# Kernel tuning notes

Measured on AMD Instinct MI355X. Metric: run time of the kernel, lower is better.

## Reference

```python
import jax, jax.numpy as jnp
import numpy as np

EPISODES = 1_000_000


def setup_inputs() -> dict:
    key = jax.random.key(0)
    x = jax.random.normal(key, (1, EPISODES, 2), dtype=jnp.float32)
    return {"x": x}


def _rx_2x2(t):
    # expm(-i * t * X) = cos(t) I - i sin(t) X  (closed form for Pauli-X rotation)
    c = jnp.cos(t).astype(jnp.complex64)
    s = (-1j * jnp.sin(t).astype(jnp.complex64))
    row0 = jnp.stack([c, s], axis=-1)
    row1 = jnp.stack([s, c], axis=-1)
    return jnp.stack([row0, row1], axis=-2)  # (..., 2, 2)


def reference(x):
    # x: (1, E, 2) float32 -> angles a (qubit 1, X(x)I) and b (qubit 2, I(x)X)
    cnot = jnp.array([[1, 0, 0, 0],
                      [0, 1, 0, 0],
                      [0, 0, 0, 1],
                      [0, 0, 1, 0]], dtype=jnp.complex64)
    a = x[..., 0]  # (1, E)
    b = x[..., 1]  # (1, E)
    # sx1 = X(x)I and sx2 = I(x)X commute, so
    # expm(-i (a*sx1 + b*sx2)) = Rx(a) (x) Rx(b)  -- exact, replaces generic expm.
    Ra = _rx_2x2(a)  # (1, E, 2, 2)
    Rb = _rx_2x2(b)  # (1, E, 2, 2)
    # Kronecker product -> (1, E, 4, 4) complex64
    Rx = (Ra[..., :, None, :, None] * Rb[..., None, :, None, :]).reshape(
        a.shape[0], a.shape[1], 4, 4)
    propagator = jnp.einsum('iq,beqp->beip', cnot, Rx)  # (1, E, 4, 4)
    state_out = propagator[..., 0]                      # column 0 -> (1, E, 4)
    probabilities = jnp.square(jnp.abs(state_out)).astype(jnp.float32)
    logits = jnp.log(probabilities)                     # tf.log(prob) for multinomial
    # Vectorized categorical sampling over all episodes (replaces per-episode loop)
    skey = jax.random.key(42)
    choice = jax.random.categorical(skey, logits, axis=-1)  # (1, E) int
    # original: one_hot((1,1)) stacked on axis=1 -> (1, E, 1, 4)
    measurement = jax.nn.one_hot(choice, 4, dtype=jnp.float32)[:, :, None, :]
    return measurement
```

## Files before the change

kernel.cpp:

```cpp
#include <hip/hip_runtime.h>
#include <stdint.h>
#include <math.h>


#define N_EP 1000000

typedef float v2f __attribute__((ext_vector_type(2)));
#define V2(c) ((v2f){(c), (c)})

__device__ __forceinline__ uint32_t rotl32(uint32_t x, int d) {
  return (x << d) | (x >> (32 - d));
}

__device__ __forceinline__ void threefry(uint32_t x0, uint32_t x1,
                                         uint32_t& o0, uint32_t& o1) {
  const uint32_t k0 = 0u;
  const uint32_t k1 = 42u;
  const uint32_t k2 = (0u ^ 42u ^ 0x1BD11BDAu);
  x0 += k0; x1 += k1;
#define R4A { x0 += x1; x1 = rotl32(x1,13); x1 ^= x0; \
              x0 += x1; x1 = rotl32(x1,15); x1 ^= x0; \
              x0 += x1; x1 = rotl32(x1,26); x1 ^= x0; \
              x0 += x1; x1 = rotl32(x1, 6); x1 ^= x0; }
#define R4B { x0 += x1; x1 = rotl32(x1,17); x1 ^= x0; \
              x0 += x1; x1 = rotl32(x1,29); x1 ^= x0; \
              x0 += x1; x1 = rotl32(x1,16); x1 ^= x0; \
              x0 += x1; x1 = rotl32(x1,24); x1 ^= x0; }
  R4A; x0 += k1; x1 += k2 + 1u;
  R4B; x0 += k2; x1 += k0 + 2u;
  R4A; x0 += k0; x1 += k1 + 3u;
  R4B; x0 += k1; x1 += k2 + 4u;
  R4A; x0 += k2; x1 += k0 + 5u;
#undef R4A
#undef R4B
  o0 = x0; o1 = x1;
}

__device__ __forceinline__ v2f logf_xla2(v2f input) {
#pragma clang fp contract(off)
  const float kMinNorm = __uint_as_float(0x00800000u);
  uint32_t ubx = __float_as_uint(fmaxf(input.x, kMinNorm));
  uint32_t uby = __float_as_uint(fmaxf(input.y, kMinNorm));
  v2f e;
  e.x = (float)((int)(ubx >> 23) - 126);
  e.y = (float)((int)(uby >> 23) - 126);
  v2f x;
  x.x = __uint_as_float((ubx & 0x807fffffu) | 0x3f000000u);
  x.y = __uint_as_float((uby & 0x807fffffu) | 0x3f000000u);
  const float kSqrtHf = 0.707106781186547524f;
  bool mx = x.x < kSqrtHf;
  bool my = x.y < kSqrtHf;
  v2f tmp;
  tmp.x = mx ? x.x : 0.0f;
  tmp.y = my ? x.y : 0.0f;
  e.x = e.x - (mx ? 1.0f : 0.0f);
  e.y = e.y - (my ? 1.0f : 0.0f);
  x = x - V2(1.0f);
  x = x + tmp;
  v2f z = x * x;
  v2f y = V2(7.0376836292E-2f);
  y = y * x + V2(-1.1514610310E-1f);
  y = y * x + V2( 1.1676998740E-1f);
  y = y * x + V2(-1.2420140846E-1f);
  y = y * x + V2( 1.4249322787E-1f);
  y = y * x + V2(-1.6668057665E-1f);
  y = y * x + V2( 2.0000714765E-1f);
  y = y * x + V2(-2.4999993993E-1f);
  y = y * x + V2( 3.3333331174E-1f);
  y = y * x;
  y = y * z;
  y = e * V2(-2.12194440e-4f) + y;
  y = z * V2(-0.5f) + y;
  x = x + y;
  x = e * V2(0.693359375f) + x;
  if (input.x == 0.0f) x.x = -__builtin_inff();
  if (input.y == 0.0f) x.y = -__builtin_inff();
  return x;
}

__device__ __forceinline__ void sincosf_cr(float xf, float* sp, float* cp) {
  double x = (double)xf;
  double dn = __builtin_rint(x * 6.36619772367581382433e-01);
  int q = (int)dn;
  const double pio2_1  = 1.57079632673412561417e+00;
  const double pio2_1t = 6.07710050650619224932e-11;
  double r = fma(-dn, pio2_1, x);
  r = fma(-dn, pio2_1t, r);
  double z = r * r;
  double w = z * z;
  const double S1 = -1.66666666666666324348e-01;
  const double S2 =  8.33333333332248946124e-03;
  const double S3 = -1.98412698298579493134e-04;
  const double S4 =  2.75573137070700676789e-06;
  const double S5 = -2.50507602534068634195e-08;
  const double S6 =  1.58969099521155010221e-10;
  double rs = S2 + z * (S3 + z * S4) + z * w * (S5 + z * S6);
  double sinr = r + r * (z * (S1 + z * rs));
  const double C1 =  4.16666666666666019037e-02;
  const double C2 = -1.38888888888741095749e-03;
  const double C3 =  2.48015872894767294178e-05;
  const double C4 = -2.75573143513906633035e-07;
  const double C5 =  2.08757232129817482790e-09;
  const double C6 = -1.13596475577881948265e-11;
  double rc = z * (C1 + z * (C2 + z * C3)) + w * w * (C4 + z * (C5 + z * C6));
  double hz = 0.5 * z;
  double ww = 1.0 - hz;
  double cosr = ww + (((1.0 - ww) - hz) + z * rc);
  bool swap = q & 1;
  double s0 = swap ? cosr : sinr;
  double c0 = swap ? sinr : cosr;
  if (q & 2) s0 = -s0;
  if ((q + 1) & 2) c0 = -c0;
  *sp = (float)s0;
  *cp = (float)c0;
}

__device__ __forceinline__ v2f u2_from_bits(uint32_t b0, uint32_t b1) {
#pragma clang fp contract(off)
  const float tiny = 1.17549435e-38f;
  v2f f;
  f.x = __uint_as_float((b0 >> 9) | 0x3F800000u);
  f.y = __uint_as_float((b1 >> 9) | 0x3F800000u);
  f = f - V2(1.0f);
  f = f + V2(tiny);
  v2f u;
  u.x = fmaxf(tiny, f.x);
  u.y = fmaxf(tiny, f.y);
  return u;
}

__device__ __forceinline__ v2f gumbel2(uint32_t b0, uint32_t b1) {
  v2f u = u2_from_bits(b0, b1);
  v2f inner = logf_xla2(u);
  v2f outer = logf_xla2(-inner);
  return -outer;
}

__global__ __launch_bounds__(256) void qcat_kernel(const float* __restrict__ x,
                                                   float* __restrict__ out) {
  int t = blockIdx.x * blockDim.x + threadIdx.x;
  if (t >= N_EP) return;

  uint32_t bits[4];
  uint32_t base = 4u * (uint32_t)t;
#pragma unroll
  for (int c = 0; c < 4; ++c) {
    uint32_t o0, o1;
    threefry(0u, base + (uint32_t)c, o0, o1);
    bits[c] = o0 ^ o1;
  }

  float2 ab = ((const float2*)x)[t];
  float ca, sa, cb, sb;
  sincosf_cr(ab.x, &sa, &ca);
  sincosf_cr(ab.y, &sb, &cb);

  {
#pragma clang fp contract(off)
    v2f m0 = {ca, ca}, n0 = {cb, sb};
    v2f m1 = {sa, sa}, n1 = {sb, cb};
    v2f t01 = m0 * n0;
    v2f t23 = m1 * n1;
    v2f p01 = t01 * t01;
    v2f p23 = t23 * t23;

    v2f lp01 = logf_xla2(p01);
    v2f lp23 = logf_xla2(p23);
    v2f g01 = gumbel2(bits[0], bits[1]);
    v2f g23 = gumbel2(bits[2], bits[3]);
    v2f y01 = lp01 + g01;
    v2f y23 = lp23 + g23;

    int best = 0; float bv = y01.x;
    if (y01.y > bv) { bv = y01.y; best = 1; }
    if (y23.x > bv) { bv = y23.x; best = 2; }
    if (y23.y > bv) { bv = y23.y; best = 3; }
    float4 o;
    o.x = (best == 0) ? 1.0f : 0.0f;
    o.y = (best == 1) ? 1.0f : 0.0f;
    o.z = (best == 2) ? 1.0f : 0.0f;
    o.w = (best == 3) ? 1.0f : 0.0f;
    ((float4*)out)[t] = o;
  }
}

extern "C" void kernel_launch(void* const* d_in, const int* in_sizes, int n_in,
                              void* d_out, int out_size, void* d_ws, size_t ws_size,
                              hipStream_t stream) {
  const float* x = (const float*)d_in[0];
  float* out = (float*)d_out;
  dim3 block(256);
  dim3 grid((N_EP + 255) / 256);
  hipLaunchKernelGGL(qcat_kernel, grid, block, 0, stream, x, out);
}
```

Baseline: 78.58 us.

## Use fast hardware transcendentals with error-bounded fallback to exact path

Computes sin/cos and logs with the hardware approximate instructions, estimates an error bound for each logit, and accepts the argmax when the winning margin exceeds twice that bound. Episodes with a small margin or denormal probabilities fall back to a non-inlined bit-exact path that uses double-precision sincos and the XLA log polynomial. This removes the costly double-precision trig and polynomial logs from most threads. The cost is divergence and extra registers for the rare fallback, and correctness depends on the error bound actually holding.

After: 72.60 us. -7.6%, faster.

```diff
diff --git a/kernel.cpp b/kernel.cpp
--- a/kernel.cpp
+++ b/kernel.cpp
@@ -35,6 +35,7 @@
 #undef R4B
   o0 = x0; o1 = x1;
 }
+
 
 __device__ __forceinline__ v2f logf_xla2(v2f input) {
 #pragma clang fp contract(off)
@@ -115,6 +116,13 @@
   *cp = (float)c0;
 }
 
+__device__ __forceinline__ float u_from_bits(uint32_t b) {
+#pragma clang fp contract(off)
+  const float tiny = 1.17549435e-38f;
+  float f = __uint_as_float((b >> 9) | 0x3F800000u) - 1.0f;
+  return fmaxf(tiny, f + tiny);
+}
+
 __device__ __forceinline__ v2f u2_from_bits(uint32_t b0, uint32_t b1) {
 #pragma clang fp contract(off)
   const float tiny = 1.17549435e-38f;
@@ -136,6 +144,36 @@
   return -outer;
 }
 
+__device__ __noinline__ int episode_exact(float a, float b,
+                                          const uint32_t bits[4]) {
+#pragma clang fp contract(off)
+  float ca, sa, cb, sb;
+  sincosf_cr(a, &sa, &ca);
+  sincosf_cr(b, &sb, &cb);
+  v2f m0 = {ca, ca}, n0 = {cb, sb};
+  v2f m1 = {sa, sa}, n1 = {sb, cb};
+  v2f t01 = m0 * n0;
+  v2f t23 = m1 * n1;
+  v2f p01 = t01 * t01;
+  v2f p23 = t23 * t23;
+  v2f y01 = logf_xla2(p01) + gumbel2(bits[0], bits[1]);
+  v2f y23 = logf_xla2(p23) + gumbel2(bits[2], bits[3]);
+  int best = 0; float bv = y01.x;
+  if (y01.y > bv) { bv = y01.y; best = 1; }
+  if (y23.x > bv) { bv = y23.x; best = 2; }
+  if (y23.y > bv) { bv = y23.y; best = 3; }
+  return best;
+}
+
+
+__device__ __forceinline__ void fast_gumbel(uint32_t b, float* g, float* rtg) {
+  const float LN2 = 0.6931471805599453f;
+  float u = u_from_bits(b);
+  float tg = -(LN2 * __builtin_amdgcn_logf(u));
+  *g = -(LN2 * __builtin_amdgcn_logf(tg));
+  *rtg = __builtin_amdgcn_rcpf(tg);
+}
+
 __global__ __launch_bounds__(256) void qcat_kernel(const float* __restrict__ x,
                                                    float* __restrict__ out) {
   int t = blockIdx.x * blockDim.x + threadIdx.x;
@@ -151,37 +189,67 @@
   }
 
   float2 ab = ((const float2*)x)[t];
-  float ca, sa, cb, sb;
-  sincosf_cr(ab.x, &sa, &ca);
-  sincosf_cr(ab.y, &sb, &cb);
-
-  {
-#pragma clang fp contract(off)
-    v2f m0 = {ca, ca}, n0 = {cb, sb};
-    v2f m1 = {sa, sa}, n1 = {sb, cb};
-    v2f t01 = m0 * n0;
-    v2f t23 = m1 * n1;
-    v2f p01 = t01 * t01;
-    v2f p23 = t23 * t23;
-
-    v2f lp01 = logf_xla2(p01);
-    v2f lp23 = logf_xla2(p23);
-    v2f g01 = gumbel2(bits[0], bits[1]);
-    v2f g23 = gumbel2(bits[2], bits[3]);
-    v2f y01 = lp01 + g01;
-    v2f y23 = lp23 + g23;
-
-    int best = 0; float bv = y01.x;
-    if (y01.y > bv) { bv = y01.y; best = 1; }
-    if (y23.x > bv) { bv = y23.x; best = 2; }
-    if (y23.y > bv) { bv = y23.y; best = 3; }
-    float4 o;
-    o.x = (best == 0) ? 1.0f : 0.0f;
-    o.y = (best == 1) ? 1.0f : 0.0f;
-    o.z = (best == 2) ? 1.0f : 0.0f;
-    o.w = (best == 3) ? 1.0f : 0.0f;
-    ((float4*)out)[t] = o;
+
+  const float INV2PI = 0.15915494309189535f;
+  const float LN2 = 0.6931471805599453f;
+  float fra = __builtin_amdgcn_fractf(ab.x * INV2PI);
+  float frb = __builtin_amdgcn_fractf(ab.y * INV2PI);
+  float saf = __builtin_amdgcn_sinf(fra);
+  float caf = __builtin_amdgcn_cosf(fra);
+  float sbf = __builtin_amdgcn_sinf(frb);
+  float cbf = __builtin_amdgcn_cosf(frb);
+  float a0 = caf * cbf, a1 = caf * sbf, a2 = saf * sbf, a3 = saf * cbf;
+  float p0 = a0 * a0, p1 = a1 * a1, p2 = a2 * a2, p3 = a3 * a3;
+  float lp0 = LN2 * __builtin_amdgcn_logf(p0);
+  float lp1 = LN2 * __builtin_amdgcn_logf(p1);
+  float lp2 = LN2 * __builtin_amdgcn_logf(p2);
+  float lp3 = LN2 * __builtin_amdgcn_logf(p3);
+  float g0, g1, g2, g3, rtg0, rtg1, rtg2, rtg3;
+  fast_gumbel(bits[0], &g0, &rtg0);
+  fast_gumbel(bits[1], &g1, &rtg1);
+  fast_gumbel(bits[2], &g2, &rtg2);
+  fast_gumbel(bits[3], &g3, &rtg3);
+  float y0 = lp0 + g0, y1 = lp1 + g1, y2 = lp2 + g2, y3 = lp3 + g3;
+
+  const float K = 1.52587890625e-5f;
+  float rta0 = __builtin_amdgcn_rcpf(fabsf(a0));
+  float rta1 = __builtin_amdgcn_rcpf(fabsf(a1));
+  float rta2 = __builtin_amdgcn_rcpf(fabsf(a2));
+  float rta3 = __builtin_amdgcn_rcpf(fabsf(a3));
+  float E0 = K * (fabsf(lp0) + fabsf(g0) + rtg0 + rta0 + 4.0f);
+  float E1 = K * (fabsf(lp1) + fabsf(g1) + rtg1 + rta1 + 4.0f);
+  float E2 = K * (fabsf(lp2) + fabsf(g2) + rtg2 + rta2 + 4.0f);
+  float E3 = K * (fabsf(lp3) + fabsf(g3) + rtg3 + rta3 + 4.0f);
+  float Emax = fmaxf(fmaxf(E0, E1), fmaxf(E2, E3));
+
+  int   i01 = (y1 > y0) ? 1 : 0;
+  float m01 = i01 ? y1 : y0;
+  float s01 = i01 ? y0 : y1;
+  int   i23 = (y3 > y2) ? 3 : 2;
+  float m23 = i23 == 3 ? y3 : y2;
+  float s23 = i23 == 3 ? y2 : y3;
+  bool  sw  = m23 > m01;
+  int   top = sw ? i23 : i01;
+  float tv  = sw ? m23 : m01;
+  float sv  = fmaxf(sw ? m01 : m23, sw ? s23 : s01);
+  float margin = tv - sv;
+
+  float pmin = fminf(fminf(p0, p1), fminf(p2, p3));
+  bool safe = (margin > 2.0f * Emax) && (pmin >= 1.17549435e-38f);
+
+  int best;
+  if (safe) {
+    best = top;
+  } else {
+    best = episode_exact(ab.x, ab.y, bits);
   }
+
+  float4 o;
+  o.x = (best == 0) ? 1.0f : 0.0f;
+  o.y = (best == 1) ? 1.0f : 0.0f;
+  o.z = (best == 2) ? 1.0f : 0.0f;
+  o.w = (best == 3) ? 1.0f : 0.0f;
+  ((float4*)out)[t] = o;
 }
 
 extern "C" void kernel_launch(void* const* d_in, const int* in_sizes, int n_in,
```
